# Kernel optimization log

Hardware: AMD Instinct MI355X
Metric: run time of the kernel (lower is better)

## Reference

```python
import jax, jax.numpy as jnp
import numpy as np

B, W, N, L = 64, 256, 128, 64


def setup_inputs() -> dict:
    key = jax.random.key(0)
    k1, k2, k3 = jax.random.split(key, 3)
    x = jax.random.normal(k1, (B, W, L), dtype=jnp.float32)
    shapelets = jax.random.normal(k2, (N, L), dtype=jnp.float32)
    cls_w = jax.random.normal(k3, (1, N), dtype=jnp.float32) * 0.1
    cls_b = jnp.zeros((1,), dtype=jnp.float32)
    return {"x": x, "shapelets": shapelets, "cls_w": cls_w, "cls_b": cls_b}


def reference(x, shapelets, cls_w, cls_b):
    # diffs: [B, W, N, L] broadcast subtract
    diffs = x[:, :, None, :] - shapelets[None, None, :, :]
    # L2 norm over shapelet-length axis -> [B, W, N]
    discrim = jnp.sqrt(jnp.sum(diffs * diffs, axis=3))
    # min over windows -> [B, N]
    min_discrim = jnp.min(discrim, axis=1)
    # tiny classifier: Linear(N, 1) + sigmoid -> [B, 1]
    logits = min_discrim @ cls_w.T + cls_b
    return jax.nn.sigmoid(logits)
```

## Files before the change

kernel.cpp:

```cpp
#include <hip/hip_runtime.h>
#include <cfloat>
#include <cmath>

constexpr int B = 64;
constexpr int W = 256;
constexpr int N = 128;
constexpr int L = 64;

template <int NCHUNKS>
__global__ __launch_bounds__(256) void shapelet_min_kernel(
    const float* __restrict__ x, const float* __restrict__ shp,
    float* __restrict__ part) {
  constexpr int WPB = W / NCHUNKS;
  constexpr int NV4 = WPB * L / 4;
  __shared__ float xs[WPB * L];
  __shared__ float xnorm_s[WPB];
  __shared__ float comb[N];

  const int b = blockIdx.x / NCHUNKS;
  const int c = blockIdx.x % NCHUNKS;
  const int tid = threadIdx.x;
  const int n = tid & (N - 1);
  const int wslot = tid >> 7;

  const float4* xg =
      (const float4*)(x + ((size_t)b * W + (size_t)c * WPB) * L);
  float4* xls = (float4*)xs;

  if constexpr (NV4 == 256) {
    float4 v = xg[tid];
    xls[tid] = v;
    float p = v.x * v.x + v.y * v.y + v.z * v.z + v.w * v.w;
    p += __shfl_xor(p, 8, 16);
    p += __shfl_xor(p, 4, 16);
    p += __shfl_xor(p, 2, 16);
    p += __shfl_xor(p, 1, 16);
    if ((tid & 15) == 0) xnorm_s[tid >> 4] = p;
  } else {
    if (tid < WPB) xnorm_s[tid] = 0.f;
    __syncthreads();
    for (int i = tid; i < NV4; i += 256) {
      float4 v = xg[i];
      xls[i] = v;
      float p = v.x * v.x + v.y * v.y + v.z * v.z + v.w * v.w;
      atomicAdd(&xnorm_s[i >> 4], p);
    }
  }

  float s[L];
  {
    const float4* sg = (const float4*)(shp + (size_t)n * L);
#pragma unroll
    for (int i = 0; i < L / 4; ++i) {
      float4 v = sg[i];
      s[4 * i + 0] = v.x;
      s[4 * i + 1] = v.y;
      s[4 * i + 2] = v.z;
      s[4 * i + 3] = v.w;
    }
  }

  __syncthreads();

  float best = FLT_MAX;
  const int w0 = wslot * (WPB / 2);
  for (int wi = 0; wi < WPB / 2; ++wi) {
    const float* xr = xs + (size_t)(w0 + wi) * L;
    float a0 = 0.f, a1 = 0.f, a2 = 0.f, a3 = 0.f;
#pragma unroll
    for (int l = 0; l < L; l += 4) {
      float4 xv = *(const float4*)(xr + l);
      a0 = fmaf(xv.x, s[l + 0], a0);
      a1 = fmaf(xv.y, s[l + 1], a1);
      a2 = fmaf(xv.z, s[l + 2], a2);
      a3 = fmaf(xv.w, s[l + 3], a3);
    }
    float dot = (a0 + a1) + (a2 + a3);
    best = fminf(best, fmaf(-2.f, dot, xnorm_s[w0 + wi]));
  }

  __syncthreads();
  if (wslot == 1) comb[n] = best;
  __syncthreads();
  if (wslot == 0) {
    part[((size_t)b * NCHUNKS + c) * N + n] = fminf(best, comb[n]);
  }
}

template <int NCHUNKS>
__global__ __launch_bounds__(128) void shapelet_head_kernel(
    const float* __restrict__ part, const float* __restrict__ shp,
    const float* __restrict__ cls_w, const float* __restrict__ cls_b,
    float* __restrict__ out) {
  const int b = blockIdx.x;
  const int n = threadIdx.x;

  float m = FLT_MAX;
#pragma unroll
  for (int c = 0; c < NCHUNKS; ++c)
    m = fminf(m, part[((size_t)b * NCHUNKS + c) * N + n]);

  float sn = 0.f;
  {
    const float4* sg = (const float4*)(shp + (size_t)n * L);
#pragma unroll
    for (int i = 0; i < L / 4; ++i) {
      float4 v = sg[i];
      sn = fmaf(v.x, v.x, sn);
      sn = fmaf(v.y, v.y, sn);
      sn = fmaf(v.z, v.z, sn);
      sn = fmaf(v.w, v.w, sn);
    }
  }

  float d2 = fmaxf(m + sn, 0.f);
  float v = sqrtf(d2) * cls_w[n];

#pragma unroll
  for (int off = 32; off > 0; off >>= 1) v += __shfl_down(v, off, 64);

  __shared__ float red[2];
  if ((n & 63) == 0) red[n >> 6] = v;
  __syncthreads();
  if (n == 0) {
    float z = red[0] + red[1] + cls_b[0];
    out[b] = 1.0f / (1.0f + expf(-z));
  }
}

template <int NCHUNKS>
static void launch_impl(const float* x, const float* shp, const float* cls_w,
                        const float* cls_b, float* out, float* part,
                        hipStream_t stream) {
  shapelet_min_kernel<NCHUNKS><<<B * NCHUNKS, 256, 0, stream>>>(x, shp, part);
  shapelet_head_kernel<NCHUNKS>
      <<<B, 128, 0, stream>>>(part, shp, cls_w, cls_b, out);
}

extern "C" void kernel_launch(void* const* d_in, const int* in_sizes, int n_in,
                              void* d_out, int out_size, void* d_ws,
                              size_t ws_size, hipStream_t stream) {
  const float* x = (const float*)d_in[0];
  const float* shp = (const float*)d_in[1];
  const float* cls_w = (const float*)d_in[2];
  const float* cls_b = (const float*)d_in[3];
  float* out = (float*)d_out;
  float* part = (float*)d_ws;

  const size_t per_chunk = (size_t)B * N * sizeof(float);
  if (ws_size >= 16 * per_chunk) {
    launch_impl<16>(x, shp, cls_w, cls_b, out, part, stream);
  } else if (ws_size >= 8 * per_chunk) {
    launch_impl<8>(x, shp, cls_w, cls_b, out, part, stream);
  } else if (ws_size >= 4 * per_chunk) {
    launch_impl<4>(x, shp, cls_w, cls_b, out, part, stream);
  } else {
    launch_impl<1>(x, shp, cls_w, cls_b, out, part, stream);
  }
}
```

Before: 71.84 us.

## Fuse min and head kernels via atomic min and last-block reduction

Replaces the two-kernel launch (partial min per chunk, then head) with one fused kernel. Each block atomically merges its per-shapelet minimum into a per-batch buffer using an order-preserving unsigned encoding, and the last block to finish, found through a global counter, computes the classifier head for all batches. This removes the second kernel launch and the partial-buffer round trip. It adds a memset launch, global atomics, and a serial tail where one block handles the whole head.

Measured after the change: 135.8 us. 89.1% more time.

```diff
diff --git a/kernel.cpp b/kernel.cpp
--- a/kernel.cpp
+++ b/kernel.cpp
@@ -6,6 +6,130 @@
 constexpr int W = 256;
 constexpr int N = 128;
 constexpr int L = 64;
+
+__device__ __forceinline__ unsigned enc_min(float f) {
+  unsigned u = __float_as_uint(f);
+  return (u & 0x80000000u) ? u : ~(u | 0x80000000u);
+}
+__device__ __forceinline__ float dec_min(unsigned m) {
+  unsigned k = ~m;
+  return (k & 0x80000000u) ? __uint_as_float(k & 0x7FFFFFFFu)
+                           : __uint_as_float(~k);
+}
+
+__global__ __launch_bounds__(256) void shapelet_fused_kernel(
+    const float* __restrict__ x, const float* __restrict__ shp,
+    const float* __restrict__ cls_w, const float* __restrict__ cls_b,
+    unsigned* __restrict__ part, unsigned* __restrict__ counter,
+    float* __restrict__ out) {
+  constexpr int WPB = 16;
+  __shared__ float xs[WPB * L];
+  __shared__ float xnorm_s[WPB];
+  __shared__ float comb[N];
+  __shared__ unsigned last_flag;
+
+  const int b = blockIdx.x >> 4;
+  const int c = blockIdx.x & 15;
+  const int tid = threadIdx.x;
+  const int n = tid & (N - 1);
+  const int wslot = tid >> 7;
+
+  {
+    const float4* xg =
+        (const float4*)(x + ((size_t)b * W + (size_t)c * WPB) * L);
+    float4 v = xg[tid];
+    ((float4*)xs)[tid] = v;
+    float p = v.x * v.x + v.y * v.y + v.z * v.z + v.w * v.w;
+    p += __shfl_xor(p, 8, 16);
+    p += __shfl_xor(p, 4, 16);
+    p += __shfl_xor(p, 2, 16);
+    p += __shfl_xor(p, 1, 16);
+    if ((tid & 15) == 0) xnorm_s[tid >> 4] = p;
+  }
+
+  float s[L];
+  {
+    const float4* sg = (const float4*)(shp + (size_t)n * L);
+#pragma unroll
+    for (int i = 0; i < L / 4; ++i) {
+      float4 v = sg[i];
+      s[4 * i + 0] = v.x;
+      s[4 * i + 1] = v.y;
+      s[4 * i + 2] = v.z;
+      s[4 * i + 3] = v.w;
+    }
+  }
+
+  __syncthreads();
+
+  float best = FLT_MAX;
+  const int w0 = wslot * 8;
+  for (int wi = 0; wi < 8; ++wi) {
+    const float* xr = xs + (size_t)(w0 + wi) * L;
+    float a0 = 0.f, a1 = 0.f, a2 = 0.f, a3 = 0.f;
+#pragma unroll
+    for (int l = 0; l < L; l += 4) {
+      float4 xv = *(const float4*)(xr + l);
+      a0 = fmaf(xv.x, s[l + 0], a0);
+      a1 = fmaf(xv.y, s[l + 1], a1);
+      a2 = fmaf(xv.z, s[l + 2], a2);
+      a3 = fmaf(xv.w, s[l + 3], a3);
+    }
+    best = fminf(best, fmaf(-2.f, (a0 + a1) + (a2 + a3), xnorm_s[w0 + wi]));
+  }
+
+  __syncthreads();
+  if (wslot == 1) comb[n] = best;
+  __syncthreads();
+  if (wslot == 0) {
+    atomicMax(&part[(size_t)b * N + n], enc_min(fminf(best, comb[n])));
+  }
+
+  __threadfence();
+  if (tid == 0) {
+    unsigned old = atomicAdd(counter, 1u);
+    last_flag = (old == (unsigned)(B * 16 - 1)) ? 1u : 0u;
+  }
+  __syncthreads();
+  if (last_flag == 0) return;
+  __threadfence();
+
+  __shared__ float sn_s[N], w_s[N], psum[256];
+  if (tid < N) {
+    const float4* sg = (const float4*)(shp + (size_t)tid * L);
+    float sn = 0.f;
+#pragma unroll
+    for (int i = 0; i < L / 4; ++i) {
+      float4 v = sg[i];
+      sn = fmaf(v.x, v.x, sn);
+      sn = fmaf(v.y, v.y, sn);
+      sn = fmaf(v.z, v.z, sn);
+      sn = fmaf(v.w, v.w, sn);
+    }
+    sn_s[tid] = sn;
+    w_s[tid] = cls_w[tid];
+  }
+  __syncthreads();
+
+  {
+    const int bb = tid >> 2, q = tid & 3;
+    float acc = 0.f;
+#pragma unroll 4
+    for (int j = 0; j < 32; ++j) {
+      const int nn = q * 32 + j;
+      unsigned m = atomicMax(&part[(size_t)bb * N + nn], 0u);
+      float d2 = fmaxf(dec_min(m) + sn_s[nn], 0.f);
+      acc = fmaf(sqrtf(d2), w_s[nn], acc);
+    }
+    psum[tid] = acc;
+  }
+  __syncthreads();
+  if (tid < B) {
+    float z = psum[4 * tid] + psum[4 * tid + 1] + psum[4 * tid + 2] +
+              psum[4 * tid + 3] + cls_b[0];
+    out[tid] = 1.0f / (1.0f + expf(-z));
+  }
+}
 
 template <int NCHUNKS>
 __global__ __launch_bounds__(256) void shapelet_min_kernel(
@@ -23,45 +147,29 @@
   const int n = tid & (N - 1);
   const int wslot = tid >> 7;
 
-  const float4* xg =
-      (const float4*)(x + ((size_t)b * W + (size_t)c * WPB) * L);
-  float4* xls = (float4*)xs;
-
-  if constexpr (NV4 == 256) {
-    float4 v = xg[tid];
-    xls[tid] = v;
-    float p = v.x * v.x + v.y * v.y + v.z * v.z + v.w * v.w;
-    p += __shfl_xor(p, 8, 16);
-    p += __shfl_xor(p, 4, 16);
-    p += __shfl_xor(p, 2, 16);
-    p += __shfl_xor(p, 1, 16);
-    if ((tid & 15) == 0) xnorm_s[tid >> 4] = p;
-  } else {
-    if (tid < WPB) xnorm_s[tid] = 0.f;
-    __syncthreads();
+  if (tid < WPB) xnorm_s[tid] = 0.f;
+  __syncthreads();
+  {
+    const float4* xg =
+        (const float4*)(x + ((size_t)b * W + (size_t)c * WPB) * L);
     for (int i = tid; i < NV4; i += 256) {
       float4 v = xg[i];
-      xls[i] = v;
-      float p = v.x * v.x + v.y * v.y + v.z * v.z + v.w * v.w;
-      atomicAdd(&xnorm_s[i >> 4], p);
-    }
-  }
-
+      ((float4*)xs)[i] = v;
+      atomicAdd(&xnorm_s[i >> 4],
+                v.x * v.x + v.y * v.y + v.z * v.z + v.w * v.w);
+    }
+  }
   float s[L];
   {
     const float4* sg = (const float4*)(shp + (size_t)n * L);
 #pragma unroll
     for (int i = 0; i < L / 4; ++i) {
       float4 v = sg[i];
-      s[4 * i + 0] = v.x;
-      s[4 * i + 1] = v.y;
-      s[4 * i + 2] = v.z;
-      s[4 * i + 3] = v.w;
-    }
-  }
-
-  __syncthreads();
-
+      s[4 * i + 0] = v.x; s[4 * i + 1] = v.y;
+      s[4 * i + 2] = v.z; s[4 * i + 3] = v.w;
+    }
+  }
+  __syncthreads();
   float best = FLT_MAX;
   const int w0 = wslot * (WPB / 2);
   for (int wi = 0; wi < WPB / 2; ++wi) {
@@ -75,16 +183,13 @@
       a2 = fmaf(xv.z, s[l + 2], a2);
       a3 = fmaf(xv.w, s[l + 3], a3);
     }
-    float dot = (a0 + a1) + (a2 + a3);
-    best = fminf(best, fmaf(-2.f, dot, xnorm_s[w0 + wi]));
-  }
-
+    best = fminf(best, fmaf(-2.f, (a0 + a1) + (a2 + a3), xnorm_s[w0 + wi]));
+  }
   __syncthreads();
   if (wslot == 1) comb[n] = best;
   __syncthreads();
-  if (wslot == 0) {
+  if (wslot == 0)
     part[((size_t)b * NCHUNKS + c) * N + n] = fminf(best, comb[n]);
-  }
 }
 
 template <int NCHUNKS>
@@ -94,12 +199,10 @@
     float* __restrict__ out) {
   const int b = blockIdx.x;
   const int n = threadIdx.x;
-
   float m = FLT_MAX;
 #pragma unroll
   for (int c = 0; c < NCHUNKS; ++c)
     m = fminf(m, part[((size_t)b * NCHUNKS + c) * N + n]);
-
   float sn = 0.f;
   {
     const float4* sg = (const float4*)(shp + (size_t)n * L);
@@ -112,13 +215,9 @@
       sn = fmaf(v.w, v.w, sn);
     }
   }
-
-  float d2 = fmaxf(m + sn, 0.f);
-  float v = sqrtf(d2) * cls_w[n];
-
+  float v = sqrtf(fmaxf(m + sn, 0.f)) * cls_w[n];
 #pragma unroll
   for (int off = 32; off > 0; off >>= 1) v += __shfl_down(v, off, 64);
-
   __shared__ float red[2];
   if ((n & 63) == 0) red[n >> 6] = v;
   __syncthreads();
@@ -126,15 +225,6 @@
     float z = red[0] + red[1] + cls_b[0];
     out[b] = 1.0f / (1.0f + expf(-z));
   }
-}
-
-template <int NCHUNKS>
-static void launch_impl(const float* x, const float* shp, const float* cls_w,
-                        const float* cls_b, float* out, float* part,
-                        hipStream_t stream) {
-  shapelet_min_kernel<NCHUNKS><<<B * NCHUNKS, 256, 0, stream>>>(x, shp, part);
-  shapelet_head_kernel<NCHUNKS>
-      <<<B, 128, 0, stream>>>(part, shp, cls_w, cls_b, out);
 }
 
 extern "C" void kernel_launch(void* const* d_in, const int* in_sizes, int n_in,
@@ -145,16 +235,18 @@
   const float* cls_w = (const float*)d_in[2];
   const float* cls_b = (const float*)d_in[3];
   float* out = (float*)d_out;
-  float* part = (float*)d_ws;
-
-  const size_t per_chunk = (size_t)B * N * sizeof(float);
-  if (ws_size >= 16 * per_chunk) {
-    launch_impl<16>(x, shp, cls_w, cls_b, out, part, stream);
-  } else if (ws_size >= 8 * per_chunk) {
-    launch_impl<8>(x, shp, cls_w, cls_b, out, part, stream);
-  } else if (ws_size >= 4 * per_chunk) {
-    launch_impl<4>(x, shp, cls_w, cls_b, out, part, stream);
+
+  const size_t fused_bytes = (size_t)(B * N + 1) * sizeof(unsigned);
+  if (ws_size >= fused_bytes) {
+    unsigned* part = (unsigned*)d_ws;
+    unsigned* counter = part + (size_t)B * N;
+    hipMemsetAsync(d_ws, 0, fused_bytes, stream);
+    shapelet_fused_kernel<<<B * 16, 256, 0, stream>>>(x, shp, cls_w, cls_b,
+                                                      part, counter, out);
   } else {
-    launch_impl<1>(x, shp, cls_w, cls_b, out, part, stream);
-  }
-}
+    float* part = (float*)d_ws;
+    shapelet_min_kernel<1><<<B, 256, 0, stream>>>(x, shp, part);
+    shapelet_head_kernel<1><<<B, 128, 0, stream>>>(part, shp, cls_w, cls_b,
+                                                   out);
+  }
+}
```
